# Optimization experiments

Measured on AMD Instinct MI355X. Metric: run time of the kernel, lower is better.

## Reference

```python
import jax, jax.numpy as jnp
import numpy as np

B, L, C, H = 4, 2048, 1024, 16
D = C // H
MAX_SCALE_MUL = float(np.log(100.0))
EPS = 1e-12


def setup_inputs() -> dict:
    key = jax.random.key(0)
    ks = jax.random.split(key, 7)
    return {
        "x": jax.random.normal(ks[0], (B, L, C), dtype=jnp.float32),
        "W_qkv": jax.random.normal(ks[1], (3 * C, C), dtype=jnp.float32) * (C ** -0.5),
        "q_bias": jax.random.normal(ks[2], (C,), dtype=jnp.float32) * 0.02,
        "v_bias": jax.random.normal(ks[3], (C,), dtype=jnp.float32) * 0.02,
        "scale_mul_log": jnp.full((1, H, 1, 1), np.log(4.0), dtype=jnp.float32),
        "W_proj": jax.random.normal(ks[4], (C, C), dtype=jnp.float32) * (C ** -0.5),
        "b_proj": jax.random.normal(ks[5], (C,), dtype=jnp.float32) * 0.02,
    }


def reference(x, W_qkv, q_bias, v_bias, scale_mul_log, W_proj, b_proj):
    Bb, Ll, Cc = x.shape
    # fused QKV projection with bias = cat(q_bias, zeros, v_bias)
    bias = jnp.concatenate([q_bias, jnp.zeros_like(q_bias), v_bias])
    qkv = (x @ W_qkv.T + bias).reshape(Bb, Ll, 3, H, D)
    q, k, v = (jnp.transpose(qkv[:, :, i], (0, 2, 1, 3)) for i in range(3))  # [B,H,L,D]
    # L2-norm attention: normalize q,k; learned per-head scale on q (clamped)
    scale_mul = jnp.exp(jnp.minimum(scale_mul_log, MAX_SCALE_MUL))  # [1,H,1,1]
    q = q / jnp.maximum(jnp.linalg.norm(q, axis=-1, keepdims=True), EPS) * scale_mul
    k = k / jnp.maximum(jnp.linalg.norm(k, axis=-1, keepdims=True), EPS)
    # SDPA with scale=1 (attn_l2_norm path), no mask, no dropout (eval)
    scores = jnp.einsum("bhqd,bhkd->bhqk", q, k)
    attn = jax.nn.softmax(scores, axis=-1)
    out = jnp.einsum("bhqk,bhkd->bhqd", attn, v)
    out = jnp.transpose(out, (0, 2, 1, 3)).reshape(Bb, Ll, Cc)
    return out @ W_proj.T + b_proj
```

## Files before the change

### kernel.cpp

```cpp
#include <hip/hip_runtime.h>
#include <hip/hip_bf16.h>


typedef __attribute__((ext_vector_type(8))) short bf16x8;
typedef __attribute__((ext_vector_type(16))) float f32x16;

#define MAXLOG 4.60517018598809f
#define LOG2E  1.4426950408889634f

__device__ __forceinline__ float bf2f(unsigned short u) {
    union { unsigned int i; float f; } v; v.i = ((unsigned int)u) << 16; return v.f;
}
__device__ __forceinline__ unsigned short f2bf(float f) {
    union { float f; unsigned int i; } v; v.f = f;
    unsigned int x = v.i;
    return (unsigned short)((x + 0x7FFFu + ((x >> 16) & 1u)) >> 16);
}
__device__ __forceinline__ unsigned fbits(float f) {
    union { float f; unsigned u; } v; v.f = f; return v.u;
}
__device__ __forceinline__ bf16x8 pack8(const float* __restrict__ p) {
    float4 a = *(const float4*)p;
    float4 b = *(const float4*)(p + 4);
    bf16x8 r;
    r[0] = (short)f2bf(a.x); r[1] = (short)f2bf(a.y);
    r[2] = (short)f2bf(a.z); r[3] = (short)f2bf(a.w);
    r[4] = (short)f2bf(b.x); r[5] = (short)f2bf(b.y);
    r[6] = (short)f2bf(b.z); r[7] = (short)f2bf(b.w);
    return r;
}
__device__ __forceinline__ void gload_lds16(const void* g, void* l) {
    __builtin_amdgcn_global_load_lds((const __attribute__((address_space(1))) void*)g,
                                     (__attribute__((address_space(3))) void*)l, 16, 0, 0);
}

__global__ __launch_bounds__(256) void k_prep(
    const float* __restrict__ x, const float* __restrict__ Wqkv,
    const float* __restrict__ Wp, const float* __restrict__ qbia,
    const float* __restrict__ vbia,
    unsigned short* __restrict__ xb, unsigned short* __restrict__ Wqkvb,
    unsigned short* __restrict__ Wpb, float* __restrict__ bias3)
{
    int i = blockIdx.x * 256 + threadIdx.x;
    if (i < 1048576) {
        *(bf16x8*)&xb[(long)i * 8] = pack8(&x[(long)i * 8]);
    } else if (i < 1441792) {
        int j = i - 1048576;
        *(bf16x8*)&Wqkvb[(long)j * 8] = pack8(&Wqkv[(long)j * 8]);
    } else if (i < 1572864) {
        int j = i - 1441792;
        *(bf16x8*)&Wpb[(long)j * 8] = pack8(&Wp[(long)j * 8]);
    } else if (i < 1573248) {
        int j = (i - 1572864) * 8;
        for (int u = 0; u < 8; ++u) {
            int n = j + u;
            float v = 0.0f;
            if (n < 1024) v = qbia[n];
            else if (n >= 2048) v = vbia[n - 2048];
            bias3[n] = v;
        }
    }
}

template<bool OUT_F32, bool KNORM>
__global__ __launch_bounds__(256) void k_gemm_lds(
    const unsigned short* __restrict__ A, const unsigned short* __restrict__ Bh,
    const float* __restrict__ bias, void* __restrict__ Cp, int N, int K)
{
    __shared__ unsigned short As[2][128 * 32];
    __shared__ unsigned short Bs[2][128 * 32];
    const int t = threadIdx.x, wave = t >> 6, lane = t & 63;
    const int m32 = lane & 31, half = lane >> 5;
    const int bm = blockIdx.x * 128, bn = blockIdx.y * 128;
    const int wr = (wave >> 1) * 64, wc = (wave & 1) * 64;
    f32x16 acc[2][2] = {};

    const int srow = lane >> 2;
    const int scol = (((lane & 3) ^ ((lane >> 3) & 3))) * 8;
    const int c0 = wave * 2, c1 = wave * 2 + 1;
    const long ga0 = (long)(bm + c0 * 16 + srow) * K + scol;
    const long ga1 = (long)(bm + c1 * 16 + srow) * K + scol;
    const long gb0 = (long)(bn + c0 * 16 + srow) * K + scol;
    const long gb1 = (long)(bn + c1 * 16 + srow) * K + scol;

    const int swz = (m32 >> 1) & 3;

    gload_lds16(&A[ga0], &As[0][c0 * 512]);
    gload_lds16(&A[ga1], &As[0][c1 * 512]);
    gload_lds16(&Bh[gb0], &Bs[0][c0 * 512]);
    gload_lds16(&Bh[gb1], &Bs[0][c1 * 512]);
    __syncthreads();

    int cur = 0;
    for (int kt = 0; kt < K; kt += 32) {
        const int nxt = kt + 32;
        if (nxt < K) {
            gload_lds16(&A[ga0 + nxt], &As[cur ^ 1][c0 * 512]);
            gload_lds16(&A[ga1 + nxt], &As[cur ^ 1][c1 * 512]);
            gload_lds16(&Bh[gb0 + nxt], &Bs[cur ^ 1][c0 * 512]);
            gload_lds16(&Bh[gb1 + nxt], &Bs[cur ^ 1][c1 * 512]);
        }
        bf16x8 af[2][2], bfr[2][2];
        for (int mt = 0; mt < 2; ++mt)
            for (int f = 0; f < 2; ++f)
                af[mt][f] = *(const bf16x8*)&As[cur][(wr + mt * 32 + m32) * 32 +
                                                    (((f * 2 + half) ^ swz) * 8)];
        for (int nt = 0; nt < 2; ++nt)
            for (int f = 0; f < 2; ++f)
                bfr[nt][f] = *(const bf16x8*)&Bs[cur][(wc + nt * 32 + m32) * 32 +
                                                     (((f * 2 + half) ^ swz) * 8)];
        for (int f = 0; f < 2; ++f)
            for (int mt = 0; mt < 2; ++mt)
                for (int nt = 0; nt < 2; ++nt)
                    acc[mt][nt] = __builtin_amdgcn_mfma_f32_32x32x16_bf16(
                        af[mt][f], bfr[nt][f], acc[mt][nt], 0, 0, 0);
        __syncthreads();
        cur ^= 1;
    }

    const bool isk = KNORM && (bn >= 1024) && (bn < 2048);
    const float bv0 = bias[bn + wc + m32];
    const float bv1 = bias[bn + wc + 32 + m32];
    for (int mt = 0; mt < 2; ++mt)
        for (int r = 0; r < 16; ++r) {
            int gm = bm + wr + mt * 32 + (r & 3) + 8 * (r >> 2) + 4 * half;
            float inv = 1.0f;
            if (isk) {
                float ss = acc[mt][0][r] * acc[mt][0][r]
                         + acc[mt][1][r] * acc[mt][1][r];
                ss += __shfl_xor(ss, 1, 64);
                ss += __shfl_xor(ss, 2, 64);
                ss += __shfl_xor(ss, 4, 64);
                ss += __shfl_xor(ss, 8, 64);
                ss += __shfl_xor(ss, 16, 64);
                inv = 1.0f / fmaxf(sqrtf(ss), 1e-12f);
            }
            for (int nt = 0; nt < 2; ++nt) {
                int gn = bn + wc + nt * 32 + m32;
                float val = acc[mt][nt][r] + (nt ? bv1 : bv0);
                if (isk) val *= inv;
                if (OUT_F32) ((float*)Cp)[(long)gm * N + gn] = val;
                else ((unsigned short*)Cp)[(long)gm * N + gn] = f2bf(val);
            }
        }
}

__global__ __launch_bounds__(256) void k_prep_v(
    const unsigned short* __restrict__ qkv, unsigned short* __restrict__ vT)
{
    __shared__ unsigned short Vsh[64 * 72];
    const int t = threadIdx.x;
    const int bh = blockIdx.y, l0 = blockIdx.x * 64;
    const int h = bh & 15, b = bh >> 4;
    const int ll = t >> 2, c16 = (t & 3) * 16;
    const long rowbase = (long)(b * 2048 + l0 + ll) * 3072;

    *(bf16x8*)&Vsh[ll * 72 + c16]     = *(const bf16x8*)&qkv[rowbase + 2048 + h * 64 + c16];
    *(bf16x8*)&Vsh[ll * 72 + c16 + 8] = *(const bf16x8*)&qkv[rowbase + 2048 + h * 64 + c16 + 8];
    __syncthreads();
    const int d = t >> 2, ls = (t & 3) * 16;
    unsigned short tmp[16];
    for (int j = 0; j < 16; ++j) tmp[j] = Vsh[(ls + j) * 72 + d];
    long dst = (long)(bh * 64 + d) * 2048 + l0 + ls;
    *(bf16x8*)&vT[dst]     = *(bf16x8*)&tmp[0];
    *(bf16x8*)&vT[dst + 8] = *(bf16x8*)&tmp[8];
}

__global__ __launch_bounds__(256, 2) void k_attn32(
    const unsigned short* __restrict__ qkv,
    const unsigned short* __restrict__ vT, const float* __restrict__ sml,
    unsigned short* __restrict__ attn)
{
    __shared__ unsigned short Ks[2][64 * 72];
    __shared__ unsigned short Vs[2][64 * 72];
    const int t = threadIdx.x, wave = t >> 6, lane = t & 63;
    const int m32 = lane & 31, half = lane >> 5;
    const int wg = blockIdx.x;
    const int logical = (wg & 7) * 64 + (wg >> 3);
    const int bh = logical >> 3, qblk = logical & 7;
    const int h = bh & 15, b = bh >> 4;
    const int q0 = qblk * 256 + wave * 64;
    const float scale = __expf(fminf(sml[h], MAXLOG));
    const float c2 = scale * LOG2E;

    const int qd = m32 >> 2, lo = qd & 3;
    const int prow = ((((lo == 1) || (lo == 2)) ? (qd ^ 3) : qd) << 2) | (m32 & 3);

    bf16x8 aqA[4], aqB[4];
    {
        long base = (long)(b * 2048 + q0 + m32) * 3072 + h * 64;
        float e[32]; float ss = 0.f;
        for (int f = 0; f < 4; ++f) {
            aqA[f] = *(const bf16x8*)&qkv[base + f * 16 + half * 8];
            for (int j = 0; j < 8; ++j) { float x = bf2f((unsigned short)aqA[f][j]); e[f * 8 + j] = x; ss += x * x; }
        }
        ss += __shfl_xor(ss, 32, 64);
        float rs = (scale * LOG2E) / fmaxf(sqrtf(ss), 1e-12f);
        for (int f = 0; f < 4; ++f)
            for (int j = 0; j < 8; ++j) aqA[f][j] = (short)f2bf(e[f * 8 + j] * rs);
    }
    {
        long base = (long)(b * 2048 + q0 + 32 + m32) * 3072 + h * 64;
        float e[32]; float ss = 0.f;
        for (int f = 0; f < 4; ++f) {
            aqB[f] = *(const bf16x8*)&qkv[base + f * 16 + half * 8];
            for (int j = 0; j < 8; ++j) { float x = bf2f((unsigned short)aqB[f][j]); e[f * 8 + j] = x; ss += x * x; }
        }
        ss += __shfl_xor(ss, 32, 64);
        float rs = (scale * LOG2E) / fmaxf(sqrtf(ss), 1e-12f);
        for (int f = 0; f < 4; ++f)
            for (int j = 0; j < 8; ++j) aqB[f][j] = (short)f2bf(e[f * 8 + j] * rs);
    }

    f32x16 oA0 = {}, oA1 = {}, lA = {};
    f32x16 oB0 = {}, oB1 = {}, lB = {};
    bf16x8 ones; for (int i = 0; i < 8; ++i) ones[i] = (short)0x3F80;
    const int sr = t >> 2, sc = (t & 3) * 16;
    const long kqrow = (long)(b * 2048) * 3072 + 1024 + h * 64;
    const long vbase = (long)bh * 64 * 2048;

#define LOADT(kt) \
    kpA = *(const bf16x8*)&qkv[kqrow + (long)((kt) + sr) * 3072 + sc];      \
    kpB = *(const bf16x8*)&qkv[kqrow + (long)((kt) + sr) * 3072 + sc + 8];  \
    vpA = *(const bf16x8*)&vT[vbase + (long)sr * 2048 + (kt) + sc];         \
    vpB = *(const bf16x8*)&vT[vbase + (long)sr * 2048 + (kt) + sc + 8];

#define STORET(buf) \
    *(bf16x8*)&Ks[buf][sr * 72 + sc]     = kpA;  \
    *(bf16x8*)&Ks[buf][sr * 72 + sc + 8] = kpB;  \
    *(bf16x8*)&Vs[buf][sr * 72 + sc]     = vpA;  \
    *(bf16x8*)&Vs[buf][sr * 72 + sc + 8] = vpB;

#define SCORE(AQ, AP0, AP1, KF0, KF1, KF2, KF3, SUB) \
    {                                                                                      \
        f32x16 s = {};                                                                     \
        s = __builtin_amdgcn_mfma_f32_32x32x16_bf16(KF0, AQ[0], s, 0, 0, 0);               \
        s = __builtin_amdgcn_mfma_f32_32x32x16_bf16(KF1, AQ[1], s, 0, 0, 0);               \
        s = __builtin_amdgcn_mfma_f32_32x32x16_bf16(KF2, AQ[2], s, 0, 0, 0);               \
        s = __builtin_amdgcn_mfma_f32_32x32x16_bf16(KF3, AQ[3], s, 0, 0, 0);               \
        unsigned pu[16];                                                                   \
        for (int j = 0; j < 16; ++j)                                                       \
            pu[j] = fbits(__builtin_amdgcn_exp2f(s[j] - (SUB)));                           \
        uint4 a0u, a1u;                                                                    \
        a0u.x = __builtin_amdgcn_perm(pu[1],  pu[0],  0x07060302u);                        \
        a0u.y = __builtin_amdgcn_perm(pu[3],  pu[2],  0x07060302u);                        \
        a0u.z = __builtin_amdgcn_perm(pu[5],  pu[4],  0x07060302u);                        \
        a0u.w = __builtin_amdgcn_perm(pu[7],  pu[6],  0x07060302u);                        \
        a1u.x = __builtin_amdgcn_perm(pu[9],  pu[8],  0x07060302u);                        \
        a1u.y = __builtin_amdgcn_perm(pu[11], pu[10], 0x07060302u);                        \
        a1u.z = __builtin_amdgcn_perm(pu[13], pu[12], 0x07060302u);                        \
        a1u.w = __builtin_amdgcn_perm(pu[15], pu[14], 0x07060302u);                        \
        __builtin_memcpy(&AP0, &a0u, 16); __builtin_memcpy(&AP1, &a1u, 16);                \
    }

#define ATTN_STEP(KS, VS, SUB) \
    for (int ktile = 0; ktile < 2; ++ktile) {                                              \
        const unsigned short* krow = &KS[(ktile * 32 + prow) * 72 + half * 8];             \
        bf16x8 kf0 = *(const bf16x8*)&krow[0];                                             \
        bf16x8 kf1 = *(const bf16x8*)&krow[16];                                            \
        bf16x8 kf2 = *(const bf16x8*)&krow[32];                                            \
        bf16x8 kf3 = *(const bf16x8*)&krow[48];                                            \
        bf16x8 apA0, apA1, apB0, apB1;                                                     \
        SCORE(aqA, apA0, apA1, kf0, kf1, kf2, kf3, SUB)                                    \
        SCORE(aqB, apB0, apB1, kf0, kf1, kf2, kf3, SUB)                                    \
        for (int c = 0; c < 2; ++c) {                                                      \
            bf16x8 aA = c ? apA1 : apA0;                                                   \
            bf16x8 aB = c ? apB1 : apB0;                                                   \
            bf16x8 bv0 = *(const bf16x8*)&VS[m32 * 72        + ktile * 32 + c * 16 + half * 8]; \
            bf16x8 bv1 = *(const bf16x8*)&VS[(32 + m32) * 72 + ktile * 32 + c * 16 + half * 8]; \
            oA0 = __builtin_amdgcn_mfma_f32_32x32x16_bf16(aA, bv0, oA0, 0, 0, 0);          \
            oA1 = __builtin_amdgcn_mfma_f32_32x32x16_bf16(aA, bv1, oA1, 0, 0, 0);          \
            lA  = __builtin_amdgcn_mfma_f32_32x32x16_bf16(aA, ones, lA, 0, 0, 0);          \
            oB0 = __builtin_amdgcn_mfma_f32_32x32x16_bf16(aB, bv0, oB0, 0, 0, 0);          \
            oB1 = __builtin_amdgcn_mfma_f32_32x32x16_bf16(aB, bv1, oB1, 0, 0, 0);          \
            lB  = __builtin_amdgcn_mfma_f32_32x32x16_bf16(aB, ones, lB, 0, 0, 0);          \
        }                                                                                  \
    }

#define KLOOP(SUB) \
    for (int kt = 0; kt < 2048; kt += 128) {                 \
        LOADT(kt + 64)                                       \
        ATTN_STEP(Ks[0], Vs[0], SUB)                         \
        STORET(1)                                            \
        __syncthreads();                                     \
        const bool more = (kt + 128) < 2048;                 \
        if (more) { LOADT(kt + 128) }                        \
        ATTN_STEP(Ks[1], Vs[1], SUB)                         \
        if (more) {                                          \
            STORET(0)                                        \
            __syncthreads();                                 \
        }                                                    \
    }

    bf16x8 kpA, kpB, vpA, vpB;
    LOADT(0)
    STORET(0)
    __syncthreads();

    if (c2 < 30.0f) {
        KLOOP(0.0f)
    } else {
        KLOOP(c2)
    }
#undef LOADT
#undef STORET
#undef SCORE
#undef ATTN_STEP
#undef KLOOP

    for (int r = 0; r < 16; ++r) {
        int m = (r & 3) + 8 * (r >> 2) + 4 * half;
        float invA = 1.0f / lA[r];
        long dstA = (long)(b * 2048 + q0 + m) * 1024 + h * 64;
        attn[dstA + m32]      = f2bf(oA0[r] * invA);
        attn[dstA + 32 + m32] = f2bf(oA1[r] * invA);
        float invB = 1.0f / lB[r];
        long dstB = (long)(b * 2048 + q0 + 32 + m) * 1024 + h * 64;
        attn[dstB + m32]      = f2bf(oB0[r] * invB);
        attn[dstB + 32 + m32] = f2bf(oB1[r] * invB);
    }
}

extern "C" void kernel_launch(void* const* d_in, const int* in_sizes, int n_in,
                              void* d_out, int out_size, void* d_ws, size_t ws_size,
                              hipStream_t stream) {
    const float* x    = (const float*)d_in[0];
    const float* Wqkv = (const float*)d_in[1];
    const float* qbia = (const float*)d_in[2];
    const float* vbia = (const float*)d_in[3];
    const float* sml  = (const float*)d_in[4];
    const float* Wp   = (const float*)d_in[5];
    const float* bp   = (const float*)d_in[6];

    char* ws = (char*)d_ws;
    unsigned short* qkv   = (unsigned short*)ws;
    unsigned short* Wqkvb = (unsigned short*)(ws + 50331648);
    unsigned short* vT    = (unsigned short*)(ws + 67108864);
    unsigned short* xb    = vT;
    unsigned short* attnb = (unsigned short*)(ws + 83886080);
    float*          bias3 = (float*)(ws + 100663296);
    unsigned short* Wpb   = (unsigned short*)(ws + 100679680);
    float*          out   = (float*)d_out;

    hipLaunchKernelGGL(k_prep, dim3(6146), dim3(256), 0, stream,
                       x, Wqkv, Wp, qbia, vbia, xb, Wqkvb, Wpb, bias3);
    hipLaunchKernelGGL((k_gemm_lds<false, true>), dim3(64, 24), dim3(256), 0, stream,
                       xb, Wqkvb, bias3, (void*)qkv, 3072, 1024);
    hipLaunchKernelGGL(k_prep_v, dim3(32, 64), dim3(256), 0, stream, qkv, vT);
    hipLaunchKernelGGL(k_attn32, dim3(512), dim3(256), 0, stream, qkv, vT, sml, attnb);
    hipLaunchKernelGGL((k_gemm_lds<true, false>), dim3(64, 8), dim3(256), 0, stream,
                       attnb, Wpb, bp, (void*)out, 1024, 1024);
}
```

Baseline: 279.7 us.

## Pre-tile bf16 operands into swizzled chunk layout and single-buffer GEMM LDS

The conversion kernel now writes x and both weight matrices in a blocked 16x32 tile order with the LDS swizzle baked in, so each wave's global-to-LDS load reads one contiguous 1 KB chunk. The GEMM gains template flags to address these packed operands and switches from double-buffered to single-buffered LDS with syncs around each load. This aims at more coalesced global loads and lower LDS use (higher occupancy), at the cost of losing prefetch overlap between loads and MFMA. The epilogue is also restructured to apply bias before the k-normalization.

```diff
diff --git a/kernel.cpp b/kernel.cpp
--- a/kernel.cpp
+++ b/kernel.cpp
@@ -43,13 +43,25 @@
 {
     int i = blockIdx.x * 256 + threadIdx.x;
     if (i < 1048576) {
-        *(bf16x8*)&xb[(long)i * 8] = pack8(&x[(long)i * 8]);
+        int chunk = i >> 6, l = i & 63;
+        int r16 = chunk >> 5, kc = chunk & 31;
+        int rin = l >> 2, cq = (l & 3) ^ ((rin >> 1) & 3);
+        long src = (long)(r16 * 16 + rin) * 1024 + kc * 32 + cq * 8;
+        *(bf16x8*)&xb[(long)i * 8] = pack8(&x[src]);
     } else if (i < 1441792) {
         int j = i - 1048576;
-        *(bf16x8*)&Wqkvb[(long)j * 8] = pack8(&Wqkv[(long)j * 8]);
+        int chunk = j >> 6, l = j & 63;
+        int r16 = chunk >> 5, kc = chunk & 31;
+        int rin = l >> 2, cq = (l & 3) ^ ((rin >> 1) & 3);
+        long src = (long)(r16 * 16 + rin) * 1024 + kc * 32 + cq * 8;
+        *(bf16x8*)&Wqkvb[(long)j * 8] = pack8(&Wqkv[src]);
     } else if (i < 1572864) {
         int j = i - 1441792;
-        *(bf16x8*)&Wpb[(long)j * 8] = pack8(&Wp[(long)j * 8]);
+        int chunk = j >> 6, l = j & 63;
+        int r16 = chunk >> 5, kc = chunk & 31;
+        int rin = l >> 2, cq = (l & 3) ^ ((rin >> 1) & 3);
+        long src = (long)(r16 * 16 + rin) * 1024 + kc * 32 + cq * 8;
+        *(bf16x8*)&Wpb[(long)j * 8] = pack8(&Wp[src]);
     } else if (i < 1573248) {
         int j = (i - 1572864) * 8;
         for (int u = 0; u < 8; ++u) {
@@ -62,60 +74,56 @@
     }
 }
 
-template<bool OUT_F32, bool KNORM>
+template<bool OUT_F32, bool KNORM, bool PA, bool PB>
 __global__ __launch_bounds__(256) void k_gemm_lds(
     const unsigned short* __restrict__ A, const unsigned short* __restrict__ Bh,
     const float* __restrict__ bias, void* __restrict__ Cp, int N, int K)
 {
-    __shared__ unsigned short As[2][128 * 32];
-    __shared__ unsigned short Bs[2][128 * 32];
+    __shared__ unsigned short As[128 * 32];
+    __shared__ unsigned short Bs[128 * 32];
     const int t = threadIdx.x, wave = t >> 6, lane = t & 63;
     const int m32 = lane & 31, half = lane >> 5;
     const int bm = blockIdx.x * 128, bn = blockIdx.y * 128;
     const int wr = (wave >> 1) * 64, wc = (wave & 1) * 64;
     f32x16 acc[2][2] = {};
 
+    const int KC = K >> 5;
     const int srow = lane >> 2;
     const int scol = (((lane & 3) ^ ((lane >> 3) & 3))) * 8;
     const int c0 = wave * 2, c1 = wave * 2 + 1;
-    const long ga0 = (long)(bm + c0 * 16 + srow) * K + scol;
-    const long ga1 = (long)(bm + c1 * 16 + srow) * K + scol;
-    const long gb0 = (long)(bn + c0 * 16 + srow) * K + scol;
-    const long gb1 = (long)(bn + c1 * 16 + srow) * K + scol;
+    long a0, a1, b0, b1;
+    if (PA) { a0 = (long)((bm >> 4) + c0) * KC * 512 + lane * 8;
+              a1 = (long)((bm >> 4) + c1) * KC * 512 + lane * 8; }
+    else    { a0 = (long)(bm + c0 * 16 + srow) * K + scol;
+              a1 = (long)(bm + c1 * 16 + srow) * K + scol; }
+    if (PB) { b0 = (long)((bn >> 4) + c0) * KC * 512 + lane * 8;
+              b1 = (long)((bn >> 4) + c1) * KC * 512 + lane * 8; }
+    else    { b0 = (long)(bn + c0 * 16 + srow) * K + scol;
+              b1 = (long)(bn + c1 * 16 + srow) * K + scol; }
 
     const int swz = (m32 >> 1) & 3;
 
-    gload_lds16(&A[ga0], &As[0][c0 * 512]);
-    gload_lds16(&A[ga1], &As[0][c1 * 512]);
-    gload_lds16(&Bh[gb0], &Bs[0][c0 * 512]);
-    gload_lds16(&Bh[gb1], &Bs[0][c1 * 512]);
-    __syncthreads();
-
-    int cur = 0;
     for (int kt = 0; kt < K; kt += 32) {
-        const int nxt = kt + 32;
-        if (nxt < K) {
-            gload_lds16(&A[ga0 + nxt], &As[cur ^ 1][c0 * 512]);
-            gload_lds16(&A[ga1 + nxt], &As[cur ^ 1][c1 * 512]);
-            gload_lds16(&Bh[gb0 + nxt], &Bs[cur ^ 1][c0 * 512]);
-            gload_lds16(&Bh[gb1 + nxt], &Bs[cur ^ 1][c1 * 512]);
-        }
+        __syncthreads();
+        gload_lds16(&A[a0 + (PA ? kt * 16 : kt)], &As[c0 * 512]);
+        gload_lds16(&A[a1 + (PA ? kt * 16 : kt)], &As[c1 * 512]);
+        gload_lds16(&Bh[b0 + (PB ? kt * 16 : kt)], &Bs[c0 * 512]);
+        gload_lds16(&Bh[b1 + (PB ? kt * 16 : kt)], &Bs[c1 * 512]);
+        __syncthreads();
         bf16x8 af[2][2], bfr[2][2];
         for (int mt = 0; mt < 2; ++mt)
             for (int f = 0; f < 2; ++f)
-                af[mt][f] = *(const bf16x8*)&As[cur][(wr + mt * 32 + m32) * 32 +
-                                                    (((f * 2 + half) ^ swz) * 8)];
+                af[mt][f] = *(const bf16x8*)&As[(wr + mt * 32 + m32) * 32 +
+                                                (((f * 2 + half) ^ swz) * 8)];
         for (int nt = 0; nt < 2; ++nt)
             for (int f = 0; f < 2; ++f)
-                bfr[nt][f] = *(const bf16x8*)&Bs[cur][(wc + nt * 32 + m32) * 32 +
-                                                     (((f * 2 + half) ^ swz) * 8)];
+                bfr[nt][f] = *(const bf16x8*)&Bs[(wc + nt * 32 + m32) * 32 +
+                                                 (((f * 2 + half) ^ swz) * 8)];
         for (int f = 0; f < 2; ++f)
             for (int mt = 0; mt < 2; ++mt)
                 for (int nt = 0; nt < 2; ++nt)
                     acc[mt][nt] = __builtin_amdgcn_mfma_f32_32x32x16_bf16(
                         af[mt][f], bfr[nt][f], acc[mt][nt], 0, 0, 0);
-        __syncthreads();
-        cur ^= 1;
     }
 
     const bool isk = KNORM && (bn >= 1024) && (bn < 2048);
@@ -124,23 +132,24 @@
     for (int mt = 0; mt < 2; ++mt)
         for (int r = 0; r < 16; ++r) {
             int gm = bm + wr + mt * 32 + (r & 3) + 8 * (r >> 2) + 4 * half;
-            float inv = 1.0f;
+            float v0 = acc[mt][0][r] + bv0;
+            float v1 = acc[mt][1][r] + bv1;
             if (isk) {
-                float ss = acc[mt][0][r] * acc[mt][0][r]
-                         + acc[mt][1][r] * acc[mt][1][r];
+                float ss = v0 * v0 + v1 * v1;
                 ss += __shfl_xor(ss, 1, 64);
                 ss += __shfl_xor(ss, 2, 64);
                 ss += __shfl_xor(ss, 4, 64);
                 ss += __shfl_xor(ss, 8, 64);
                 ss += __shfl_xor(ss, 16, 64);
-                inv = 1.0f / fmaxf(sqrtf(ss), 1e-12f);
+                float inv = 1.0f / fmaxf(sqrtf(ss), 1e-12f);
+                v0 *= inv; v1 *= inv;
             }
-            for (int nt = 0; nt < 2; ++nt) {
-                int gn = bn + wc + nt * 32 + m32;
-                float val = acc[mt][nt][r] + (nt ? bv1 : bv0);
-                if (isk) val *= inv;
-                if (OUT_F32) ((float*)Cp)[(long)gm * N + gn] = val;
-                else ((unsigned short*)Cp)[(long)gm * N + gn] = f2bf(val);
+            if (OUT_F32) {
+                ((float*)Cp)[(long)gm * N + bn + wc + m32]      = v0;
+                ((float*)Cp)[(long)gm * N + bn + wc + 32 + m32] = v1;
+            } else {
+                ((unsigned short*)Cp)[(long)gm * N + bn + wc + m32]      = f2bf(v0);
+                ((unsigned short*)Cp)[(long)gm * N + bn + wc + 32 + m32] = f2bf(v1);
             }
         }
 }
@@ -344,10 +353,10 @@
 
     hipLaunchKernelGGL(k_prep, dim3(6146), dim3(256), 0, stream,
                        x, Wqkv, Wp, qbia, vbia, xb, Wqkvb, Wpb, bias3);
-    hipLaunchKernelGGL((k_gemm_lds<false, true>), dim3(64, 24), dim3(256), 0, stream,
+    hipLaunchKernelGGL((k_gemm_lds<false, true, true, true>), dim3(64, 24), dim3(256), 0, stream,
                        xb, Wqkvb, bias3, (void*)qkv, 3072, 1024);
     hipLaunchKernelGGL(k_prep_v, dim3(32, 64), dim3(256), 0, stream, qkv, vT);
     hipLaunchKernelGGL(k_attn32, dim3(512), dim3(256), 0, stream, qkv, vT, sml, attnb);
-    hipLaunchKernelGGL((k_gemm_lds<true, false>), dim3(64, 8), dim3(256), 0, stream,
+    hipLaunchKernelGGL((k_gemm_lds<true, false, false, true>), dim3(64, 8), dim3(256), 0, stream,
                        attnb, Wpb, bp, (void*)out, 1024, 1024);
 }
```

After: 276.0 us. No clear change (-1.3%).
